# Kernel optimization log

Measured on AMD Instinct MI355X. Metric: run time of the kernel, lower is better.

The kernel has to match this reference:

```python
import jax, jax.numpy as jnp
import numpy as np

B, S, D, H = 2, 2048, 1024, 16
HD = D // H  # head_dim = 64


def setup_inputs() -> dict:
    key = jax.random.key(0)
    ks = jax.random.split(key, 9)
    s_in = 1.0 / np.sqrt(D)
    inp = {
        "hidden_state": jax.random.normal(ks[0], (B, S, D), dtype=jnp.float32),
        # per-head projections, stacked: [H, D, HD]
        "Wq": jax.random.uniform(ks[1], (H, D, HD), jnp.float32, -s_in, s_in),
        "bq": jax.random.uniform(ks[2], (H, HD), jnp.float32, -s_in, s_in),
        "Wk": jax.random.uniform(ks[3], (H, D, HD), jnp.float32, -s_in, s_in),
        "bk": jax.random.uniform(ks[4], (H, HD), jnp.float32, -s_in, s_in),
        "Wv": jax.random.uniform(ks[5], (H, D, HD), jnp.float32, -s_in, s_in),
        "bv": jax.random.uniform(ks[6], (H, HD), jnp.float32, -s_in, s_in),
        # output linear: [D, D]
        "Wo": jax.random.uniform(ks[7], (D, D), jnp.float32, -s_in, s_in),
        "bo": jax.random.uniform(ks[8], (D,), jnp.float32, -s_in, s_in),
    }
    return inp


def reference(hidden_state, Wq, bq, Wk, bk, Wv, bv, Wo, bo):
    # fused per-head projections: [B, H, S, HD]
    q = jnp.einsum("bsd,hde->bhse", hidden_state, Wq) + bq[None, :, None, :]
    k = jnp.einsum("bsd,hde->bhse", hidden_state, Wk) + bk[None, :, None, :]
    v = jnp.einsum("bsd,hde->bhse", hidden_state, Wv) + bv[None, :, None, :]
    scale = 1.0 / jnp.sqrt(jnp.float32(HD))
    scores = jnp.einsum("bhse,bhte->bhst", q, k) * scale  # [B, H, S, S]
    weights = jax.nn.softmax(scores, axis=-1)
    ctx = jnp.einsum("bhst,bhte->bhse", weights, v)       # [B, H, S, HD]
    # concat heads along last dim -> [B, S, D]
    ctx = jnp.transpose(ctx, (0, 2, 1, 3)).reshape(B, S, D)
    return ctx @ Wo + bo
```

## Files before the change

### kernel.cpp

```cpp
#include <hip/hip_runtime.h>
#include <hip/hip_bf16.h>
#include <math.h>

#define BB 2
#define SS 2048
#define DD 1024
#define HH 16
#define HD 64

typedef __attribute__((ext_vector_type(8))) _Float16 f16x8;
typedef __attribute__((ext_vector_type(8))) unsigned short u16x8;
typedef __attribute__((ext_vector_type(4))) float f32x4;
typedef __attribute__((ext_vector_type(4))) unsigned short u16x4;

__device__ __forceinline__ unsigned short hbits(_Float16 h) {
    union { _Float16 h; unsigned short s; } u; u.h = h; return u.s;
}

__global__ __launch_bounds__(256) void prep_convert(
    const float* __restrict__ X,
    const float* __restrict__ Wq, const float* __restrict__ Wk,
    const float* __restrict__ Wv, const float* __restrict__ Wo,
    unsigned short* __restrict__ Xh, unsigned short* __restrict__ WT)
{
    __shared__ __align__(16) unsigned short LT[64 * 68];
    const int bid = blockIdx.x;
    const int tid = threadIdx.x;

    if (bid < 2048) {
        const int base = bid * 2048 + tid * 8;
        float4 a = *(const float4*)&X[base];
        float4 b = *(const float4*)&X[base + 4];
        u16x8 o;
        o[0] = hbits((_Float16)a.x); o[1] = hbits((_Float16)a.y);
        o[2] = hbits((_Float16)a.z); o[3] = hbits((_Float16)a.w);
        o[4] = hbits((_Float16)b.x); o[5] = hbits((_Float16)b.y);
        o[6] = hbits((_Float16)b.z); o[7] = hbits((_Float16)b.w);
        *(u16x8*)&Xh[base] = o;
        return;
    }

    const int t = bid - 2048;
    const float* src;
    size_t stride;
    int outRow0, kcol0;
    if (t < 768) {
        const int nt = t >> 4, ktile = t & 15;
        const int sel = nt >> 4, hh = nt & 15;
        const float* Ws = (sel == 0) ? Wq : ((sel == 1) ? Wk : Wv);
        src = Ws + (size_t)hh * (DD * HD) + (size_t)ktile * 64 * HD;
        stride = HD;
        outRow0 = nt * 64;
        kcol0 = ktile * 64;
    } else {
        const int tt = t - 768;
        const int nt = tt & 15, ktile = tt >> 4;
        src = Wo + (size_t)ktile * 64 * DD + nt * 64;
        stride = DD;
        outRow0 = 3072 + nt * 64;
        kcol0 = ktile * 64;
    }

    const int e = tid & 63, dq = tid >> 6;
#pragma unroll
    for (int p = 0; p < 16; p++) {
        const int dl = p * 4 + dq;
        LT[e * 68 + dl] = hbits((_Float16)src[(size_t)dl * stride + e]);
    }
    __syncthreads();
    const int eo = tid >> 2, d16 = (tid & 3) * 16;
#pragma unroll
    for (int j = 0; j < 4; j++) {
        *(ushort4*)&WT[(size_t)(outRow0 + eo) * DD + kcol0 + d16 + j * 4] =
            *(const ushort4*)&LT[eo * 68 + d16 + j * 4];
    }
}

#define GBM 128
#define GBN 128
#define GBK 64

__global__ __launch_bounds__(256) void qkv_gemm(
    const unsigned short* __restrict__ Xh, const unsigned short* __restrict__ WT,
    const float* __restrict__ bq, const float* __restrict__ bk,
    const float* __restrict__ bv,
    unsigned short* __restrict__ qh, unsigned short* __restrict__ kh,
    unsigned short* __restrict__ vh, unsigned int* __restrict__ kc2)
{
    __shared__ __align__(16) unsigned short As[16 * 512];
    __shared__ __align__(16) unsigned short Bs[16 * 512];

    const int tid = threadIdx.x;
    const int m0 = blockIdx.y * GBM;
    const int n0 = blockIdx.x * GBN;
    const int lane = tid & 63;
    const int w = tid >> 6;
    const int wm = w & 1, wn = w >> 1;
    const int l15 = lane & 15, quad = lane >> 4;

    int g_off[4], l_off[4];
#pragma unroll
    for (int p = 0; p < 4; p++) {
        const int s = p * 256 + tid;
        const int c = s >> 6, j = s & 63;
        g_off[p] = ((c >> 1) * 16 + (j & 15)) * DD + (c & 1) * 32 + (j >> 4) * 8;
        l_off[p] = c * 512 + j * 8;
    }

    f32x4 acc[4][4];
#pragma unroll
    for (int i = 0; i < 4; i++)
#pragma unroll
        for (int j = 0; j < 4; j++) acc[i][j] = (f32x4){0.f, 0.f, 0.f, 0.f};

    const unsigned short* Abase = Xh + (size_t)m0 * DD;
    const unsigned short* Bbase = WT + (size_t)n0 * DD;

    for (int kt = 0; kt < DD; kt += GBK) {
        __syncthreads();
#pragma unroll
        for (int p = 0; p < 4; p++) {
            *(u16x8*)&As[l_off[p]] = *(const u16x8*)&Abase[g_off[p] + kt];
            *(u16x8*)&Bs[l_off[p]] = *(const u16x8*)&Bbase[g_off[p] + kt];
        }
        __syncthreads();
#pragma unroll
        for (int ks = 0; ks < 2; ks++) {
            f16x8 af[4], bf[4];
#pragma unroll
            for (int i = 0; i < 4; i++) {
                af[i] = *(const f16x8*)&As[((wm * 4 + i) * 2 + ks) * 512 + lane * 8];
                bf[i] = *(const f16x8*)&Bs[((wn * 4 + i) * 2 + ks) * 512 + lane * 8];
            }
#pragma unroll
            for (int ns = 0; ns < 4; ns++)
#pragma unroll
                for (int ms = 0; ms < 4; ms++)
                    acc[ms][ns] = __builtin_amdgcn_mfma_f32_16x16x32_f16(
                        af[ms], bf[ns], acc[ms][ns], 0, 0, 0);
        }
    }

    const int sel = n0 >> 10;
    const int hw = ((n0 + wn * 64) >> 6) & 15;
    const int bblk = m0 >> 11;
    const float* bias = (sel == 0) ? bq : ((sel == 1) ? bk : bv);
    unsigned short* dst = (sel == 0) ? qh : ((sel == 1) ? kh : vh);
    float wmx = 0.0f;
#pragma unroll
    for (int ms = 0; ms < 4; ms++) {
#pragma unroll
        for (int rr = 0; rr < 4; rr++) {
            const int m = m0 + wm * 64 + ms * 16 + quad * 4 + rr;
            const int s = m & (SS - 1);
            float v2 = 0.0f;
#pragma unroll
            for (int ns = 0; ns < 4; ns++) {
                const int e = ns * 16 + l15;
                const size_t ofs = (((size_t)bblk * HH + hw) * SS + s) * HD + e;
                const float val = acc[ms][ns][rr] + bias[hw * HD + e];
                if (sel == 1) v2 = fmaf(val, val, v2);
                dst[ofs] = hbits((_Float16)val);
            }
            if (sel == 1) {
                v2 += __shfl_xor(v2, 1);
                v2 += __shfl_xor(v2, 2);
                v2 += __shfl_xor(v2, 4);
                v2 += __shfl_xor(v2, 8);
                wmx = fmaxf(wmx, v2);
            }
        }
    }
    if (sel == 1) {
        wmx = fmaxf(wmx, __shfl_xor(wmx, 16));
        wmx = fmaxf(wmx, __shfl_xor(wmx, 32));
        if (lane == 0)
            atomicMax(&kc2[bblk * HH + hw], __float_as_uint(wmx));
    }
}

__global__ __launch_bounds__(256) void out_gemm(
    const unsigned short* __restrict__ Ctxh, const unsigned short* __restrict__ WoT,
    const float* __restrict__ bo, float* __restrict__ out)
{
    __shared__ __align__(16) unsigned short As[16 * 512];
    __shared__ __align__(16) unsigned short Bs[16 * 512];

    const int tid = threadIdx.x;
    const int m0 = blockIdx.y * GBM;
    const int n0 = blockIdx.x * GBN;
    const int lane = tid & 63;
    const int w = tid >> 6;
    const int wm = w & 1, wn = w >> 1;
    const int l15 = lane & 15, quad = lane >> 4;

    int g_off[4], l_off[4];
#pragma unroll
    for (int p = 0; p < 4; p++) {
        const int s = p * 256 + tid;
        const int c = s >> 6, j = s & 63;
        g_off[p] = ((c >> 1) * 16 + (j & 15)) * DD + (c & 1) * 32 + (j >> 4) * 8;
        l_off[p] = c * 512 + j * 8;
    }

    f32x4 acc[4][4];
#pragma unroll
    for (int i = 0; i < 4; i++)
#pragma unroll
        for (int j = 0; j < 4; j++) acc[i][j] = (f32x4){0.f, 0.f, 0.f, 0.f};

    const unsigned short* Abase = Ctxh + (size_t)m0 * DD;
    const unsigned short* Bbase = WoT + (size_t)n0 * DD;

    for (int kt = 0; kt < DD; kt += GBK) {
        __syncthreads();
#pragma unroll
        for (int p = 0; p < 4; p++) {
            *(u16x8*)&As[l_off[p]] = *(const u16x8*)&Abase[g_off[p] + kt];
            *(u16x8*)&Bs[l_off[p]] = *(const u16x8*)&Bbase[g_off[p] + kt];
        }
        __syncthreads();
#pragma unroll
        for (int ks = 0; ks < 2; ks++) {
            f16x8 af[4], bf[4];
#pragma unroll
            for (int i = 0; i < 4; i++) {
                af[i] = *(const f16x8*)&As[((wm * 4 + i) * 2 + ks) * 512 + lane * 8];
                bf[i] = *(const f16x8*)&Bs[((wn * 4 + i) * 2 + ks) * 512 + lane * 8];
            }
#pragma unroll
            for (int ns = 0; ns < 4; ns++)
#pragma unroll
                for (int ms = 0; ms < 4; ms++)
                    acc[ms][ns] = __builtin_amdgcn_mfma_f32_16x16x32_f16(
                        af[ms], bf[ns], acc[ms][ns], 0, 0, 0);
        }
    }

#pragma unroll
    for (int ms = 0; ms < 4; ms++) {
#pragma unroll
        for (int rr = 0; rr < 4; rr++) {
            const size_t m = (size_t)(m0 + wm * 64 + ms * 16 + quad * 4 + rr);
#pragma unroll
            for (int ns = 0; ns < 4; ns++) {
                const int n = n0 + wn * 64 + ns * 16 + l15;
                out[m * DD + n] = acc[ms][ns][rr] + bo[n];
            }
        }
    }
}

#define TQB 128
#define TKB 64
#define C1 0.1803368801111204f

__device__ __forceinline__ int swz(int row, int grp) {
    return (row << 6) + (((grp) ^ (row & 7)) << 3);
}

__global__ __launch_bounds__(256) void attn_mfma(
    const unsigned short* __restrict__ qh, const unsigned short* __restrict__ kh,
    const unsigned short* __restrict__ vh, const unsigned int* __restrict__ kc2,
    unsigned short* __restrict__ ctxh)
{
    __shared__ __align__(16) unsigned short KL [TKB * 64];
    __shared__ __align__(16) unsigned short VtL[HD * 64];
    __shared__ __align__(16) unsigned short PsL[4][32 * 64];

    const int tid  = threadIdx.x;
    const int lane = tid & 63;
    const int w    = tid >> 6;
    const int l15  = lane & 15;
    const int quad = lane >> 4;
    const int bh   = blockIdx.y;
    const int q0   = blockIdx.x * TQB;

    const float kfac = sqrtf(__uint_as_float(kc2[bh])) * 1.01f * C1;

    f16x8 qf[2][2];
    float M2[2];
#pragma unroll
    for (int msub = 0; msub < 2; msub++) {
        const unsigned short* qrow =
            qh + ((size_t)bh * SS + q0 + w * 32 + msub * 16 + l15) * HD;
        float nq2 = 0.0f;
#pragma unroll
        for (int dstep = 0; dstep < 2; dstep++) {
            qf[msub][dstep] = *(const f16x8*)&qrow[dstep * 32 + quad * 8];
#pragma unroll
            for (int j = 0; j < 8; j++) {
                const float x = (float)qf[msub][dstep][j];
                nq2 = fmaf(x, x, nq2);
            }
        }
        nq2 += __shfl_xor(nq2, 16);
        nq2 += __shfl_xor(nq2, 32);
        M2[msub] = sqrtf(nq2) * kfac;
    }

    f32x4 o[2][4];
    float lpart[2] = {0.f, 0.f};
#pragma unroll
    for (int ms = 0; ms < 2; ms++)
#pragma unroll
        for (int e = 0; e < 4; e++) o[ms][e] = (f32x4){0.f, 0.f, 0.f, 0.f};

    const int rg = tid >> 4;
    const int cg = tid & 15;
    const unsigned short* kb0 = kh + (size_t)bh * SS * HD;
    const unsigned short* vb0 = vh + (size_t)bh * SS * HD;

    for (int t = 0; t < SS / TKB; t++) {
        __syncthreads();

        const unsigned short* kb = kb0 + (size_t)t * TKB * HD;
#pragma unroll
        for (int p = 0; p < 2; p++) {
            const int idx = tid + p * 256;
            const int key = idx >> 3;
            const int g = idx & 7;
            *(u16x8*)&KL[swz(key, g)] = *(const u16x8*)&kb[key * HD + g * 8];
        }
        const unsigned short* vb = vb0 + (size_t)t * TKB * HD;
        u16x4 r0 = *(const u16x4*)&vb[(rg * 4 + 0) * HD + cg * 4];
        u16x4 r1 = *(const u16x4*)&vb[(rg * 4 + 1) * HD + cg * 4];
        u16x4 r2 = *(const u16x4*)&vb[(rg * 4 + 2) * HD + cg * 4];
        u16x4 r3 = *(const u16x4*)&vb[(rg * 4 + 3) * HD + cg * 4];
#pragma unroll
        for (int c = 0; c < 4; c++) {
            u16x4 tv = (u16x4){r0[c], r1[c], r2[c], r3[c]};
            *(u16x4*)&VtL[swz(cg * 4 + c, rg >> 1) + (rg & 1) * 4] = tv;
        }
        __syncthreads();

        f32x4 sc[2][4];
#pragma unroll
        for (int ksub = 0; ksub < 4; ksub++) {
            const int row = ksub * 16 + l15;
            f16x8 k0 = *(const f16x8*)&KL[swz(row, quad)];
            f16x8 k1 = *(const f16x8*)&KL[swz(row, 4 + quad)];
#pragma unroll
            for (int msub = 0; msub < 2; msub++) {
                f32x4 a = (f32x4){0.f, 0.f, 0.f, 0.f};
                a = __builtin_amdgcn_mfma_f32_16x16x32_f16(k0, qf[msub][0], a, 0, 0, 0);
                a = __builtin_amdgcn_mfma_f32_16x16x32_f16(k1, qf[msub][1], a, 0, 0, 0);
                sc[msub][ksub] = a;
            }
        }

#pragma unroll
        for (int msub = 0; msub < 2; msub++) {
            const int prow = msub * 16 + l15;
#pragma unroll
            for (int ksub = 0; ksub < 4; ksub++) {
                float p0 = exp2f(fmaf(sc[msub][ksub][0], C1, -M2[msub]));
                float p1 = exp2f(fmaf(sc[msub][ksub][1], C1, -M2[msub]));
                float p2 = exp2f(fmaf(sc[msub][ksub][2], C1, -M2[msub]));
                float p3 = exp2f(fmaf(sc[msub][ksub][3], C1, -M2[msub]));
                lpart[msub] += (p0 + p1) + (p2 + p3);
                u16x4 pw;
                pw[0] = hbits((_Float16)p0);
                pw[1] = hbits((_Float16)p1);
                pw[2] = hbits((_Float16)p2);
                pw[3] = hbits((_Float16)p3);
                *(u16x4*)&PsL[w][swz(prow, ksub * 2 + (quad >> 1)) + (quad & 1) * 4] = pw;
            }
        }

#pragma unroll
        for (int kj = 0; kj < 2; kj++) {
            f16x8 pa[2];
#pragma unroll
            for (int msub = 0; msub < 2; msub++)
                pa[msub] = *(const f16x8*)&PsL[w][swz(msub * 16 + l15, kj * 4 + quad)];
#pragma unroll
            for (int esub = 0; esub < 4; esub++) {
                f16x8 vr = *(const f16x8*)&VtL[swz(esub * 16 + l15, kj * 4 + quad)];
                o[0][esub] = __builtin_amdgcn_mfma_f32_16x16x32_f16(pa[0], vr, o[0][esub], 0, 0, 0);
                o[1][esub] = __builtin_amdgcn_mfma_f32_16x16x32_f16(pa[1], vr, o[1][esub], 0, 0, 0);
            }
        }
    }

    const int b = bh >> 4;
    const int h = bh & 15;
#pragma unroll
    for (int msub = 0; msub < 2; msub++) {
        float lf = lpart[msub];
        lf += __shfl_xor(lf, 16);
        lf += __shfl_xor(lf, 32);
#pragma unroll
        for (int rr = 0; rr < 4; rr++) {
            const float lr = __shfl(lf, quad * 4 + rr);
            const float linv = 1.0f / lr;
            const int row = q0 + w * 32 + msub * 16 + quad * 4 + rr;
#pragma unroll
            for (int esub = 0; esub < 4; esub++) {
                ctxh[((size_t)b * SS + row) * DD + h * HD + esub * 16 + l15] =
                    hbits((_Float16)(o[msub][esub][rr] * linv));
            }
        }
    }
}

extern "C" void kernel_launch(void* const* d_in, const int* in_sizes, int n_in,
                              void* d_out, int out_size, void* d_ws, size_t ws_size,
                              hipStream_t stream) {
    const float* X  = (const float*)d_in[0];
    const float* Wq = (const float*)d_in[1];
    const float* bq = (const float*)d_in[2];
    const float* Wk = (const float*)d_in[3];
    const float* bk = (const float*)d_in[4];
    const float* Wv = (const float*)d_in[5];
    const float* bv = (const float*)d_in[6];
    const float* Wo = (const float*)d_in[7];
    const float* bo = (const float*)d_in[8];
    float* out = (float*)d_out;

    const size_t NB2 = (size_t)4096 * 1024 * 2;
    unsigned char* w8 = (unsigned char*)d_ws;
    unsigned short* Xh   = (unsigned short*)(w8);
    unsigned short* WT   = (unsigned short*)(w8 + NB2);
    unsigned short* qh   = (unsigned short*)(w8 + 2 * NB2);
    unsigned short* kh   = (unsigned short*)(w8 + 3 * NB2);
    unsigned short* vh   = (unsigned short*)(w8 + 4 * NB2);
    unsigned short* ctxh = (unsigned short*)(w8 + 5 * NB2);
    unsigned int*   kc2  = (unsigned int*)(w8 + 6 * NB2);
    unsigned short* WoT  = WT + (size_t)3072 * 1024;

    hipMemsetAsync(kc2, 0, BB * HH * sizeof(unsigned int), stream);

    prep_convert<<<dim3(3072), 256, 0, stream>>>(X, Wq, Wk, Wv, Wo, Xh, WT);

    qkv_gemm<<<dim3(3072 / GBN, 4096 / GBM), 256, 0, stream>>>(
        Xh, WT, bq, bk, bv, qh, kh, vh, kc2);

    attn_mfma<<<dim3(SS / TQB, BB * HH), 256, 0, stream>>>(qh, kh, vh, kc2, ctxh);

    out_gemm<<<dim3(1024 / GBN, 4096 / GBM), 256, 0, stream>>>(ctxh, WoT, bo, out);
}
```

Measured before the change: 267.3 us.

## Use direct global-to-LDS loads with pre-swizzled K and pre-transposed V layouts

Switches the GEMM and attention tile loads to global_load_lds, which writes global data straight into shared memory and skips the register round trip. To make that possible, K is written already swizzled by the QKV GEMM, and a new vtrans kernel stores V transposed and swizzled per 64-key tile. The attention kernel also uses the hardware exp2 and packed f16 conversion, and computes the softmax row sums with an extra MFMA against a ones vector in place of shuffles. The costs are an extra kernel launch, an extra pass over V and more workspace. The row sums are now taken from the f16-rounded probabilities, which changes numerics slightly.

```diff
diff --git a/kernel.cpp b/kernel.cpp
--- a/kernel.cpp
+++ b/kernel.cpp
@@ -9,12 +9,49 @@
 #define HD 64
 
 typedef __attribute__((ext_vector_type(8))) _Float16 f16x8;
+typedef __attribute__((ext_vector_type(2))) __fp16 fp16x2;
 typedef __attribute__((ext_vector_type(8))) unsigned short u16x8;
 typedef __attribute__((ext_vector_type(4))) float f32x4;
 typedef __attribute__((ext_vector_type(4))) unsigned short u16x4;
 
 __device__ __forceinline__ unsigned short hbits(_Float16 h) {
     union { _Float16 h; unsigned short s; } u; u.h = h; return u.s;
+}
+
+__device__ __forceinline__ int swz(int row, int grp) {
+    return (row << 6) + (((grp) ^ (row & 7)) << 3);
+}
+
+__device__ __forceinline__ float fexp2(float x) {
+#if __has_builtin(__builtin_amdgcn_exp2f)
+    return __builtin_amdgcn_exp2f(x);
+#else
+    return exp2f(x);
+#endif
+}
+
+__device__ __forceinline__ u16x4 pack4(float p0, float p1, float p2, float p3) {
+#if __has_builtin(__builtin_amdgcn_cvt_pkrtz)
+    union { fp16x2 h[2]; u16x4 u; } pu;
+    pu.h[0] = __builtin_amdgcn_cvt_pkrtz(p0, p1);
+    pu.h[1] = __builtin_amdgcn_cvt_pkrtz(p2, p3);
+    return pu.u;
+#else
+    u16x4 r;
+    r[0] = hbits((_Float16)p0); r[1] = hbits((_Float16)p1);
+    r[2] = hbits((_Float16)p2); r[3] = hbits((_Float16)p3);
+    return r;
+#endif
+}
+
+__device__ __forceinline__ void gload_lds16(const unsigned short* g, unsigned short* l) {
+#if __has_builtin(__builtin_amdgcn_global_load_lds)
+    auto gp = (const __attribute__((address_space(1))) unsigned int*)(uintptr_t)g;
+    auto lp = (__attribute__((address_space(3))) unsigned int*)(uintptr_t)l;
+    __builtin_amdgcn_global_load_lds(gp, lp, 16, 0, 0);
+#else
+    *(u16x8*)(l + (threadIdx.x & 63) * 8) = *(const u16x8*)g;
+#endif
 }
 
 __global__ __launch_bounds__(256) void prep_convert(
@@ -76,6 +113,36 @@
     }
 }
 
+__global__ __launch_bounds__(256) void vtrans(
+    const unsigned short* __restrict__ vh, unsigned short* __restrict__ vTs)
+{
+    __shared__ __align__(16) unsigned short LT[64 * 72];
+    const int bh = blockIdx.x >> 5;
+    const int tile = blockIdx.x & 31;
+    const int tid = threadIdx.x;
+    const unsigned short* src = vh + (size_t)bh * SS * HD + (size_t)tile * 64 * HD;
+    unsigned short* dst = vTs + (size_t)bh * SS * HD + (size_t)tile * 4096;
+
+#pragma unroll
+    for (int p = 0; p < 2; p++) {
+        const int idx8 = p * 256 + tid;
+        const int key = idx8 >> 3, d8 = (idx8 & 7) * 8;
+        *(u16x8*)&LT[key * 72 + d8] = *(const u16x8*)&src[key * HD + d8];
+    }
+    __syncthreads();
+#pragma unroll
+    for (int p = 0; p < 2; p++) {
+        const int o8 = p * 256 + tid;
+        const int e = o8 >> 3, q8 = o8 & 7;
+        const int g = q8 ^ (e & 7);
+        u16x8 v;
+#pragma unroll
+        for (int j = 0; j < 8; j++)
+            v[j] = LT[(g * 8 + j) * 72 + e];
+        *(u16x8*)&dst[o8 * 8] = v;
+    }
+}
+
 #define GBM 128
 #define GBN 128
 #define GBK 64
@@ -98,13 +165,11 @@
     const int wm = w & 1, wn = w >> 1;
     const int l15 = lane & 15, quad = lane >> 4;
 
-    int g_off[4], l_off[4];
+    int g_off[4];
 #pragma unroll
     for (int p = 0; p < 4; p++) {
-        const int s = p * 256 + tid;
-        const int c = s >> 6, j = s & 63;
-        g_off[p] = ((c >> 1) * 16 + (j & 15)) * DD + (c & 1) * 32 + (j >> 4) * 8;
-        l_off[p] = c * 512 + j * 8;
+        const int c = p * 4 + w;
+        g_off[p] = ((c >> 1) * 16 + (lane & 15)) * DD + (c & 1) * 32 + (lane >> 4) * 8;
     }
 
     f32x4 acc[4][4];
@@ -120,8 +185,8 @@
         __syncthreads();
 #pragma unroll
         for (int p = 0; p < 4; p++) {
-            *(u16x8*)&As[l_off[p]] = *(const u16x8*)&Abase[g_off[p] + kt];
-            *(u16x8*)&Bs[l_off[p]] = *(const u16x8*)&Bbase[g_off[p] + kt];
+            gload_lds16(Abase + g_off[p] + kt, &As[(p * 4 + w) * 512]);
+            gload_lds16(Bbase + g_off[p] + kt, &Bs[(p * 4 + w) * 512]);
         }
         __syncthreads();
 #pragma unroll
@@ -145,7 +210,7 @@
     const int hw = ((n0 + wn * 64) >> 6) & 15;
     const int bblk = m0 >> 11;
     const float* bias = (sel == 0) ? bq : ((sel == 1) ? bk : bv);
-    unsigned short* dst = (sel == 0) ? qh : ((sel == 1) ? kh : vh);
+    const size_t bh_base = ((size_t)bblk * HH + hw) * SS * HD;
     float wmx = 0.0f;
 #pragma unroll
     for (int ms = 0; ms < 4; ms++) {
@@ -157,10 +222,17 @@
 #pragma unroll
             for (int ns = 0; ns < 4; ns++) {
                 const int e = ns * 16 + l15;
-                const size_t ofs = (((size_t)bblk * HH + hw) * SS + s) * HD + e;
                 const float val = acc[ms][ns][rr] + bias[hw * HD + e];
-                if (sel == 1) v2 = fmaf(val, val, v2);
-                dst[ofs] = hbits((_Float16)val);
+                if (sel == 0) {
+                    qh[bh_base + (size_t)s * HD + e] = hbits((_Float16)val);
+                } else if (sel == 1) {
+                    v2 = fmaf(val, val, v2);
+                    const size_t kofs = bh_base + (size_t)(s >> 6) * 4096
+                                      + swz(s & 63, e >> 3) + (e & 7);
+                    kh[kofs] = hbits((_Float16)val);
+                } else {
+                    vh[bh_base + (size_t)s * HD + e] = hbits((_Float16)val);
+                }
             }
             if (sel == 1) {
                 v2 += __shfl_xor(v2, 1);
@@ -194,13 +266,11 @@
     const int wm = w & 1, wn = w >> 1;
     const int l15 = lane & 15, quad = lane >> 4;
 
-    int g_off[4], l_off[4];
+    int g_off[4];
 #pragma unroll
     for (int p = 0; p < 4; p++) {
-        const int s = p * 256 + tid;
-        const int c = s >> 6, j = s & 63;
-        g_off[p] = ((c >> 1) * 16 + (j & 15)) * DD + (c & 1) * 32 + (j >> 4) * 8;
-        l_off[p] = c * 512 + j * 8;
+        const int c = p * 4 + w;
+        g_off[p] = ((c >> 1) * 16 + (lane & 15)) * DD + (c & 1) * 32 + (lane >> 4) * 8;
     }
 
     f32x4 acc[4][4];
@@ -216,8 +286,8 @@
         __syncthreads();
 #pragma unroll
         for (int p = 0; p < 4; p++) {
-            *(u16x8*)&As[l_off[p]] = *(const u16x8*)&Abase[g_off[p] + kt];
-            *(u16x8*)&Bs[l_off[p]] = *(const u16x8*)&Bbase[g_off[p] + kt];
+            gload_lds16(Abase + g_off[p] + kt, &As[(p * 4 + w) * 512]);
+            gload_lds16(Bbase + g_off[p] + kt, &Bs[(p * 4 + w) * 512]);
         }
         __syncthreads();
 #pragma unroll
@@ -255,13 +325,9 @@
 #define TKB 64
 #define C1 0.1803368801111204f
 
-__device__ __forceinline__ int swz(int row, int grp) {
-    return (row << 6) + (((grp) ^ (row & 7)) << 3);
-}
-
 __global__ __launch_bounds__(256) void attn_mfma(
     const unsigned short* __restrict__ qh, const unsigned short* __restrict__ kh,
-    const unsigned short* __restrict__ vh, const unsigned int* __restrict__ kc2,
+    const unsigned short* __restrict__ vTs, const unsigned int* __restrict__ kc2,
     unsigned short* __restrict__ ctxh)
 {
     __shared__ __align__(16) unsigned short KL [TKB * 64];
@@ -299,39 +365,30 @@
         M2[msub] = sqrtf(nq2) * kfac;
     }
 
-    f32x4 o[2][4];
-    float lpart[2] = {0.f, 0.f};
-#pragma unroll
-    for (int ms = 0; ms < 2; ms++)
+    f16x8 ones;
+#pragma unroll
+    for (int j = 0; j < 8; j++) ones[j] = (_Float16)1.0f;
+
+    f32x4 o[2][4], lones[2];
+#pragma unroll
+    for (int ms = 0; ms < 2; ms++) {
+        lones[ms] = (f32x4){0.f, 0.f, 0.f, 0.f};
 #pragma unroll
         for (int e = 0; e < 4; e++) o[ms][e] = (f32x4){0.f, 0.f, 0.f, 0.f};
-
-    const int rg = tid >> 4;
-    const int cg = tid & 15;
-    const unsigned short* kb0 = kh + (size_t)bh * SS * HD;
-    const unsigned short* vb0 = vh + (size_t)bh * SS * HD;
+    }
+
+    const unsigned short* kb0 = kh  + (size_t)bh * SS * HD;
+    const unsigned short* vb0 = vTs + (size_t)bh * SS * HD;
 
     for (int t = 0; t < SS / TKB; t++) {
         __syncthreads();
 
-        const unsigned short* kb = kb0 + (size_t)t * TKB * HD;
-#pragma unroll
-        for (int p = 0; p < 2; p++) {
-            const int idx = tid + p * 256;
-            const int key = idx >> 3;
-            const int g = idx & 7;
-            *(u16x8*)&KL[swz(key, g)] = *(const u16x8*)&kb[key * HD + g * 8];
-        }
-        const unsigned short* vb = vb0 + (size_t)t * TKB * HD;
-        u16x4 r0 = *(const u16x4*)&vb[(rg * 4 + 0) * HD + cg * 4];
-        u16x4 r1 = *(const u16x4*)&vb[(rg * 4 + 1) * HD + cg * 4];
-        u16x4 r2 = *(const u16x4*)&vb[(rg * 4 + 2) * HD + cg * 4];
-        u16x4 r3 = *(const u16x4*)&vb[(rg * 4 + 3) * HD + cg * 4];
-#pragma unroll
-        for (int c = 0; c < 4; c++) {
-            u16x4 tv = (u16x4){r0[c], r1[c], r2[c], r3[c]};
-            *(u16x4*)&VtL[swz(cg * 4 + c, rg >> 1) + (rg & 1) * 4] = tv;
-        }
+        const unsigned short* kb = kb0 + (size_t)t * 4096;
+        const unsigned short* vb = vb0 + (size_t)t * 4096;
+        gload_lds16(kb + tid * 8,        &KL [w * 512]);
+        gload_lds16(kb + 2048 + tid * 8, &KL [2048 + w * 512]);
+        gload_lds16(vb + tid * 8,        &VtL[w * 512]);
+        gload_lds16(vb + 2048 + tid * 8, &VtL[2048 + w * 512]);
         __syncthreads();
 
         f32x4 sc[2][4];
@@ -354,17 +411,12 @@
             const int prow = msub * 16 + l15;
 #pragma unroll
             for (int ksub = 0; ksub < 4; ksub++) {
-                float p0 = exp2f(fmaf(sc[msub][ksub][0], C1, -M2[msub]));
-                float p1 = exp2f(fmaf(sc[msub][ksub][1], C1, -M2[msub]));
-                float p2 = exp2f(fmaf(sc[msub][ksub][2], C1, -M2[msub]));
-                float p3 = exp2f(fmaf(sc[msub][ksub][3], C1, -M2[msub]));
-                lpart[msub] += (p0 + p1) + (p2 + p3);
-                u16x4 pw;
-                pw[0] = hbits((_Float16)p0);
-                pw[1] = hbits((_Float16)p1);
-                pw[2] = hbits((_Float16)p2);
-                pw[3] = hbits((_Float16)p3);
-                *(u16x4*)&PsL[w][swz(prow, ksub * 2 + (quad >> 1)) + (quad & 1) * 4] = pw;
+                const float p0 = fexp2(fmaf(sc[msub][ksub][0], C1, -M2[msub]));
+                const float p1 = fexp2(fmaf(sc[msub][ksub][1], C1, -M2[msub]));
+                const float p2 = fexp2(fmaf(sc[msub][ksub][2], C1, -M2[msub]));
+                const float p3 = fexp2(fmaf(sc[msub][ksub][3], C1, -M2[msub]));
+                *(u16x4*)&PsL[w][swz(prow, ksub * 2 + (quad >> 1)) + (quad & 1) * 4] =
+                    pack4(p0, p1, p2, p3);
             }
         }
 
@@ -374,6 +426,8 @@
 #pragma unroll
             for (int msub = 0; msub < 2; msub++)
                 pa[msub] = *(const f16x8*)&PsL[w][swz(msub * 16 + l15, kj * 4 + quad)];
+            lones[0] = __builtin_amdgcn_mfma_f32_16x16x32_f16(pa[0], ones, lones[0], 0, 0, 0);
+            lones[1] = __builtin_amdgcn_mfma_f32_16x16x32_f16(pa[1], ones, lones[1], 0, 0, 0);
 #pragma unroll
             for (int esub = 0; esub < 4; esub++) {
                 f16x8 vr = *(const f16x8*)&VtL[swz(esub * 16 + l15, kj * 4 + quad)];
@@ -387,13 +441,9 @@
     const int h = bh & 15;
 #pragma unroll
     for (int msub = 0; msub < 2; msub++) {
-        float lf = lpart[msub];
-        lf += __shfl_xor(lf, 16);
-        lf += __shfl_xor(lf, 32);
 #pragma unroll
         for (int rr = 0; rr < 4; rr++) {
-            const float lr = __shfl(lf, quad * 4 + rr);
-            const float linv = 1.0f / lr;
+            const float linv = 1.0f / lones[msub][rr];
             const int row = q0 + w * 32 + msub * 16 + quad * 4 + rr;
 #pragma unroll
             for (int esub = 0; esub < 4; esub++) {
@@ -425,18 +475,21 @@
     unsigned short* qh   = (unsigned short*)(w8 + 2 * NB2);
     unsigned short* kh   = (unsigned short*)(w8 + 3 * NB2);
     unsigned short* vh   = (unsigned short*)(w8 + 4 * NB2);
-    unsigned short* ctxh = (unsigned short*)(w8 + 5 * NB2);
-    unsigned int*   kc2  = (unsigned int*)(w8 + 6 * NB2);
+    unsigned short* vTs  = (unsigned short*)(w8 + 5 * NB2);
+    unsigned short* ctxh = (unsigned short*)(w8 + 6 * NB2);
+    unsigned int*   kc2  = (unsigned int*)(w8 + 7 * NB2);
     unsigned short* WoT  = WT + (size_t)3072 * 1024;
 
-    hipMemsetAsync(kc2, 0, BB * HH * sizeof(unsigned int), stream);
+    (void)hipMemsetAsync(kc2, 0, BB * HH * sizeof(unsigned int), stream);
 
     prep_convert<<<dim3(3072), 256, 0, stream>>>(X, Wq, Wk, Wv, Wo, Xh, WT);
 
     qkv_gemm<<<dim3(3072 / GBN, 4096 / GBM), 256, 0, stream>>>(
         Xh, WT, bq, bk, bv, qh, kh, vh, kc2);
 
-    attn_mfma<<<dim3(SS / TQB, BB * HH), 256, 0, stream>>>(qh, kh, vh, kc2, ctxh);
+    vtrans<<<dim3(BB * HH * 32), 256, 0, stream>>>(vh, vTs);
+
+    attn_mfma<<<dim3(SS / TQB, BB * HH), 256, 0, stream>>>(qh, kh, vTs, kc2, ctxh);
 
     out_gemm<<<dim3(1024 / GBN, 4096 / GBM), 256, 0, stream>>>(ctxh, WoT, bo, out);
 }
```

Result: faster. 241.3 us (-9.7%).
